# Performance work log

Measured on AMD Instinct MI355X. Metric: run time of the kernel, lower is better.

The kernel has to match this reference:

```python
import math
import jax, jax.numpy as jnp
import numpy as np

D_MODEL = 256
NUM_HEAD = 8
NUM_LEVEL = 1
KERNEL = 5
NUM_POINT = KERNEL * KERNEL
NUM_VAR = 5  # with_rotation=True
HEAD_DIM = D_MODEL // NUM_HEAD


def _kernel_indices(k=KERNEL):
    # odd kernel: linspace(-(k-1)/2, (k-1)/2, k); torch.meshgrid default 'ij'; stack([j,i])/k
    idx = jnp.linspace(-(k - 1) / 2.0, (k - 1) / 2.0, k)
    ii, jj = jnp.meshgrid(idx, idx, indexing='ij')
    return jnp.stack([jj, ii], axis=-1).reshape(-1, 2) / k  # (P, 2)


def setup_inputs() -> dict:
    key = jax.random.key(0)
    ks = jax.random.split(key, 8)
    B, LQ = 2, 4096
    Hf, Wf = 188, 188
    LV = Hf * Wf
    d = D_MODEL
    nb = NUM_LEVEL * NUM_HEAD * NUM_VAR
    na = NUM_HEAD * NUM_LEVEL * NUM_POINT
    return {
        'query': jax.random.normal(ks[0], (B, LQ, d), jnp.float32),
        'value': jax.random.normal(ks[1], (B, LV, d), jnp.float32),
        'ref_windows': jax.random.uniform(ks[2], (B, LQ, 7), jnp.float32),
        'W_box': jax.random.normal(ks[3], (nb, d), jnp.float32) * 0.02,
        'b_box': jax.random.uniform(ks[4], (nb,), jnp.float32),
        'W_attn': jax.random.normal(ks[5], (na, d), jnp.float32) * 0.02,
        'b_attn': jnp.zeros((na,), jnp.float32),
        'W_value': jax.random.normal(ks[6], (d, d), jnp.float32) * 0.02,
        'b_value': jnp.zeros((d,), jnp.float32),
        'W_out': jax.random.normal(ks[7], (d, d), jnp.float32) * 0.02,
        'b_out': jnp.zeros((d,), jnp.float32),
        'H_feat': Hf,
        'W_feat': Wf,
    }


def reference(query, value, ref_windows, W_box, b_box, W_attn, b_attn,
              W_value, b_value, W_out, b_out, H_feat, W_feat):
    B, LQ, d = query.shape
    LV = value.shape[1]
    Hh, Lv, P, Dh = NUM_HEAD, NUM_LEVEL, NUM_POINT, HEAD_DIM

    # value projection -> (B, LV, Hh, Dh)
    v = (value @ W_value.T + b_value).reshape(B, LV, Hh, Dh)

    # attention weights: softmax over (level*point) per head
    attn = jax.nn.softmax((query @ W_attn.T + b_attn).reshape(B, LQ, Hh, Lv * P), axis=-1)
    attn = attn.reshape(B, LQ, Hh, Lv, P)

    # --- _where_to_attend ---
    ob = (query @ W_box.T + b_box).reshape(B, LQ, Hh, Lv, NUM_VAR)
    rw = ref_windows[:, :, None, None, :]                    # (B,LQ,1,1,7)
    ref_boxes = rw[..., jnp.array([0, 1, 3, 4])]             # cx, cy, w, h
    ref_angles = rw[..., 6:7]
    off_boxes, off_angles = ob[..., :4], ob[..., 4:5]
    angles = (ref_angles + off_angles / 16.0) * (2.0 * math.pi)
    boxes = ref_boxes + off_boxes / 8.0 * ref_boxes[..., jnp.array([2, 3, 2, 3])]
    center = boxes[..., None, :2]                            # (B,LQ,Hh,Lv,1,2)
    size = boxes[..., None, 2:4]
    cos_a, sin_a = jnp.cos(angles), jnp.sin(angles)
    rot = jnp.stack([cos_a, -sin_a, sin_a, cos_a], axis=-1).reshape(B, LQ, Hh, Lv, 1, 2, 2)
    g = _kernel_indices() * jax.nn.relu(size)                # (B,LQ,Hh,Lv,P,2)
    grid = center + (g[..., None, :] * rot).sum(-1)          # (B,LQ,Hh,Lv,P,2), normalized [0,1]

    # --- single-level bilinear sampling (align_corners=False, zero padding) ---
    gl = grid[:, :, :, 0]                                    # (B,LQ,Hh,P,2)
    gx = gl[..., 0] * W_feat - 0.5
    gy = gl[..., 1] * H_feat - 0.5
    x0 = jnp.floor(gx)
    y0 = jnp.floor(gy)
    x0i = x0.astype(jnp.int32)
    y0i = y0.astype(jnp.int32)
    wx1 = gx - x0
    wy1 = gy - y0
    wx0 = 1.0 - wx1
    wy0 = 1.0 - wy1

    b_idx = jnp.arange(B)[:, None, None, None]
    h_idx = jnp.arange(Hh)[None, None, :, None]

    def gather(yi, xi):
        valid = (xi >= 0) & (xi < W_feat) & (yi >= 0) & (yi < H_feat)
        lin = jnp.clip(yi, 0, H_feat - 1) * W_feat + jnp.clip(xi, 0, W_feat - 1)
        return v[b_idx, lin, h_idx] * valid[..., None]       # (B,LQ,Hh,P,Dh)

    s = (gather(y0i, x0i) * (wy0 * wx0)[..., None]
         + gather(y0i, x0i + 1) * (wy0 * wx1)[..., None]
         + gather(y0i + 1, x0i) * (wy1 * wx0)[..., None]
         + gather(y0i + 1, x0i + 1) * (wy1 * wx1)[..., None])

    out_heads = (s * attn[:, :, :, 0, :, None]).sum(axis=3)  # (B,LQ,Hh,Dh)
    out = out_heads.reshape(B, LQ, Hh * Dh) @ W_out.T + b_out
    attn_w = attn.reshape(B, LQ, Hh, Lv, KERNEL, KERNEL)
    return out, attn_w
```

## Files before the change

### kernel.cpp

```cpp
#include <hip/hip_runtime.h>


typedef float floatx4 __attribute__((ext_vector_type(4)));
typedef short shortx8 __attribute__((ext_vector_type(8)));

static __device__ __forceinline__ unsigned short f2bf(float x) {
    unsigned int u = __float_as_uint(x);
    return (unsigned short)((u + 0x7fffu + ((u >> 16) & 1u)) >> 16);
}
static __device__ __forceinline__ unsigned int pack2(float a, float b) {
    return (unsigned int)f2bf(a) | ((unsigned int)f2bf(b) << 16);
}
static __device__ __forceinline__ void async16(const void* g, void* lds) {
    __builtin_amdgcn_global_load_lds(
        (const __attribute__((address_space(1))) unsigned int*)g,
        (__attribute__((address_space(3))) unsigned int*)lds, 16, 0, 0);
}

__global__ __launch_bounds__(256) void convert_kernel(
    const float* __restrict__ W_value, unsigned short* __restrict__ wvbf,
    const float* __restrict__ W_attn, const float* __restrict__ W_box,
    float* __restrict__ Wab,
    const float* __restrict__ W_out, unsigned short* __restrict__ wobf,
    const float* __restrict__ b_attn, const float* __restrict__ b_box,
    float* __restrict__ bab)
{
    const int blk = blockIdx.x, tid = threadIdx.x;
    if (blk < 16) {
        int base = blk * 1024 + tid;
#pragma unroll
        for (int k = 0; k < 4; ++k) {
            int j = base + k * 256;
            float4 f = ((const float4*)W_value)[j];
            ((uint2*)wvbf)[j] = make_uint2(pack2(f.x, f.y), pack2(f.z, f.w));
        }
    } else if (blk < 32) {
        int base = (blk - 16) * 1024 + tid;
#pragma unroll
        for (int k = 0; k < 4; ++k) {
            int j = base + k * 256;
            int row = j >> 6, col = (j & 63) * 4;
            float4 f;
            if (row < 200)      f = *(const float4*)(W_attn + (size_t)row * 256 + col);
            else if (row < 240) f = *(const float4*)(W_box + (size_t)(row - 200) * 256 + col);
            else                f = make_float4(0.f, 0.f, 0.f, 0.f);
            ((float4*)Wab)[j] = f;
        }
    } else if (blk < 48) {
        int base = (blk - 32) * 1024 + tid;
#pragma unroll
        for (int k = 0; k < 4; ++k) {
            int j = base + k * 256;
            float4 f = ((const float4*)W_out)[j];
            ((uint2*)wobf)[j] = make_uint2(pack2(f.x, f.y), pack2(f.z, f.w));
        }
    } else {
        bab[tid] = tid < 200 ? b_attn[tid] : (tid < 240 ? b_box[tid - 200] : 0.f);
    }
}

template <int OUTMODE, int AFP32, int BM>
__global__ __launch_bounds__(256) void gemm_bf16(
    const void* __restrict__ Av,
    const unsigned short* __restrict__ Bw,
    const float* __restrict__ bias,
    void* __restrict__ Cv, int M, int LV)
{
    constexpr int NI = BM / 32;
    constexpr int TI = BM / 32;
    __shared__ unsigned short As[BM * 64];
    __shared__ unsigned short Bs[128 * 64];
    const int tid = threadIdx.x;
    const int wv = tid >> 6, lane = tid & 63;
    const int lr = lane & 15, lq = lane >> 4;
    const int m0 = blockIdx.x * BM, n0 = blockIdx.y * 128;
    const int wm = wv & 1, wn = wv >> 1;
    const int srow = tid >> 3;
    const int scol = (tid & 7) * 8;

    floatx4 acc[TI][4];
#pragma unroll
    for (int i = 0; i < TI; ++i)
#pragma unroll
        for (int j = 0; j < 4; ++j) acc[i][j] = (floatx4){0.f, 0.f, 0.f, 0.f};

    for (int kc = 0; kc < 4; ++kc) {
        const int k0 = kc * 64;
        __syncthreads();
#pragma unroll
        for (int i = 0; i < 4; ++i) {
            int rb = n0 + i * 32 + srow;
            async16(Bw + (size_t)rb * 256 + k0 + scol, (char*)Bs + i * 4096 + wv * 1024);
        }
        if constexpr (AFP32) {
            const float* Af = (const float*)Av;
#pragma unroll
            for (int i = 0; i < NI; ++i) {
                int ra = m0 + i * 32 + srow; ra = ra < M ? ra : M - 1;
                const float* ap = Af + (size_t)ra * 256 + k0 + scol;
                float4 f0 = *(const float4*)ap;
                float4 f1 = *(const float4*)(ap + 4);
                uint4 pv = make_uint4(pack2(f0.x, f0.y), pack2(f0.z, f0.w),
                                      pack2(f1.x, f1.y), pack2(f1.z, f1.w));
                *(uint4*)((char*)As + i * 4096 + wv * 1024 + lane * 16) = pv;
            }
        } else {
            const unsigned short* Ab = (const unsigned short*)Av;
#pragma unroll
            for (int i = 0; i < NI; ++i) {
                int ra = m0 + i * 32 + srow; ra = ra < M ? ra : M - 1;
                async16(Ab + (size_t)ra * 256 + k0 + scol, (char*)As + i * 4096 + wv * 1024);
            }
        }
        __syncthreads();
#pragma unroll
        for (int kk = 0; kk < 64; kk += 32) {
            shortx8 af[TI], bfr[4];
#pragma unroll
            for (int t = 0; t < TI; ++t)
                af[t]  = *(const shortx8*)&As[(wm * (BM / 2) + t * 16 + lr) * 64 + kk + lq * 8];
#pragma unroll
            for (int t = 0; t < 4; ++t)
                bfr[t] = *(const shortx8*)&Bs[(wn * 64 + t * 16 + lr) * 64 + kk + lq * 8];
#pragma unroll
            for (int ti = 0; ti < TI; ++ti)
#pragma unroll
                for (int tj = 0; tj < 4; ++tj)
                    acc[ti][tj] = __builtin_amdgcn_mfma_f32_16x16x32_bf16(bfr[tj], af[ti], acc[ti][tj], 0, 0, 0);
        }
    }
#pragma unroll
    for (int ti = 0; ti < TI; ++ti) {
        int m = m0 + wm * (BM / 2) + ti * 16 + lr;
        if (m >= M) continue;
        if (OUTMODE == 0) {
            float* Crow = (float*)Cv + (size_t)m * 256;
#pragma unroll
            for (int tj = 0; tj < 4; ++tj) {
                int nb = n0 + wn * 64 + tj * 16 + lq * 4;
                float4 bv = *(const float4*)(bias + nb);
                float4 o = make_float4(acc[ti][tj][0] + bv.x, acc[ti][tj][1] + bv.y,
                                       acc[ti][tj][2] + bv.z, acc[ti][tj][3] + bv.w);
                *(float4*)(Crow + nb) = o;
            }
        } else {
            int b = m >= LV ? 1 : 0;
            int lv = m - (b ? LV : 0);
#pragma unroll
            for (int tj = 0; tj < 4; ++tj) {
                int nb = n0 + wn * 64 + tj * 16 + lq * 4;
                float4 bv = *(const float4*)(bias + nb);
                int h = nb >> 5, dh = nb & 31;
                unsigned short* dst = (unsigned short*)Cv + ((size_t)(b * 8 + h) * LV + lv) * 32 + dh;
                *(uint2*)dst = make_uint2(pack2(acc[ti][tj][0] + bv.x, acc[ti][tj][1] + bv.y),
                                          pack2(acc[ti][tj][2] + bv.z, acc[ti][tj][3] + bv.w));
            }
        }
    }
}

__global__ __launch_bounds__(256) void gemm_nt_bias(
    const float* __restrict__ A, const float* __restrict__ W,
    const float* __restrict__ bias, float* __restrict__ C, int M)
{
    const int K = 256, N = 256;
    __shared__ float As[16][68];
    __shared__ float Bs[16][68];
    int tid = threadIdx.x;
    int tcol = tid & 15, trow = tid >> 4;
    int m0 = blockIdx.x * 64, n0 = blockIdx.y * 64;
    int lr = tid >> 2, lc = (tid & 3) << 2;
    float acc[4][4] = {};
    for (int k0 = 0; k0 < K; k0 += 16) {
        int arow = m0 + lr; if (arow > M - 1) arow = M - 1;
        float4 av = *(const float4*)(A + (size_t)arow * K + k0 + lc);
        float4 wv = *(const float4*)(W + (size_t)(n0 + lr) * K + k0 + lc);
        __syncthreads();
        As[lc + 0][lr] = av.x; As[lc + 1][lr] = av.y; As[lc + 2][lr] = av.z; As[lc + 3][lr] = av.w;
        Bs[lc + 0][lr] = wv.x; Bs[lc + 1][lr] = wv.y; Bs[lc + 2][lr] = wv.z; Bs[lc + 3][lr] = wv.w;
        __syncthreads();
#pragma unroll
        for (int k = 0; k < 16; ++k) {
            float4 a4 = *(const float4*)&As[k][trow << 2];
            float4 b4 = *(const float4*)&Bs[k][tcol << 2];
            float a[4] = {a4.x, a4.y, a4.z, a4.w};
            float bb[4] = {b4.x, b4.y, b4.z, b4.w};
#pragma unroll
            for (int i = 0; i < 4; i++)
#pragma unroll
                for (int j = 0; j < 4; j++) acc[i][j] += a[i] * bb[j];
        }
    }
#pragma unroll
    for (int i = 0; i < 4; i++) {
        int m = m0 + trow * 4 + i;
        if (m >= M) continue;
#pragma unroll
        for (int j = 0; j < 4; j++) {
            int n = n0 + tcol * 4 + j;
            C[(size_t)m * N + n] = acc[i][j] + bias[n];
        }
    }
}

__global__ __launch_bounds__(256) void decode_sample_kernel(
    const unsigned short* __restrict__ v,
    const float* __restrict__ logits,
    const float* __restrict__ ref_windows,
    float* __restrict__ attn_out,
    unsigned short* __restrict__ ohbf,
    const int* __restrict__ Hf_p, const int* __restrict__ Wf_p, int LV, int LQ)
{
    __shared__ float lg[8][32];
    __shared__ float rw[8][7];
    __shared__ float prm[8][6];
    __shared__ float mxinv[8][2];
    __shared__ uint4 pk[8][25][2];

    const int lin = blockIdx.y * 16 + blockIdx.x;
    const int nc = gridDim.y;
    const int seq = lin >> 3;
    const int c = seq % nc;
    const int s = (lin & 7) + ((seq / nc) << 3);
    const int b = s >> 3, h = s & 7;
    const int tid = threadIdx.x;
    const int Hf = *Hf_p, Wf = *Wf_p;
    const size_t mbase = (size_t)b * LQ + c * 8;

    if (tid < 240) {
        int qq = tid / 30, j = tid - qq * 30;
        int col = (j < 25) ? h * 25 + j : 200 + h * 5 + (j - 25);
        lg[qq][j] = logits[(mbase + qq) * 256 + col];
    }
    if (tid < 56) {
        int qq = tid / 7, k = tid - qq * 7;
        rw[qq][k] = ref_windows[(mbase + qq) * 7 + k];
    }
    __syncthreads();

    if (tid < 8) {
        int qq = tid;
        float mx = -1e30f;
#pragma unroll
        for (int p = 0; p < 25; p++) mx = fmaxf(mx, lg[qq][p]);
        float ssum = 0.f;
#pragma unroll
        for (int p = 0; p < 25; p++) ssum += expf(lg[qq][p] - mx);
        mxinv[qq][0] = mx; mxinv[qq][1] = 1.f / ssum;
        float cx = rw[qq][0] + lg[qq][25] * 0.125f * rw[qq][3];
        float cy = rw[qq][1] + lg[qq][26] * 0.125f * rw[qq][4];
        float bw = rw[qq][3] + lg[qq][27] * 0.125f * rw[qq][3];
        float bh = rw[qq][4] + lg[qq][28] * 0.125f * rw[qq][4];
        float ang = (rw[qq][6] + lg[qq][29] * 0.0625f) * 6.283185307179586f;
        prm[qq][0] = cx; prm[qq][1] = cy;
        prm[qq][2] = fmaxf(bw, 0.f); prm[qq][3] = fmaxf(bh, 0.f);
        prm[qq][4] = cosf(ang); prm[qq][5] = sinf(ang);
    }
    __syncthreads();

    if (tid < 200) {
        int qq = tid / 25, p = tid - qq * 25;
        float a = expf(lg[qq][p] - mxinv[qq][0]) * mxinv[qq][1];
        attn_out[(mbase + qq) * 200 + h * 25 + p] = a;
        int pi = p / 5, pj = p - pi * 5;
        float g0 = (float)(pj - 2) * 0.2f * prm[qq][2];
        float g1 = (float)(pi - 2) * 0.2f * prm[qq][3];
        float ca = prm[qq][4], sa = prm[qq][5];
        float gx = (prm[qq][0] + g0 * ca - g1 * sa) * (float)Wf - 0.5f;
        float gy = (prm[qq][1] + g0 * sa + g1 * ca) * (float)Hf - 0.5f;
        float x0f = floorf(gx), y0f = floorf(gy);
        int x0 = (int)x0f, y0 = (int)y0f;
        float wx1 = gx - x0f, wy1 = gy - y0f;
        float wx0 = 1.f - wx1, wy0 = 1.f - wy1;
        int y1 = y0 + 1;
        int bx; float wl, wr;
        if (x0 >= 0 && x0 <= Wf - 2)      { bx = x0;     wl = wx0; wr = wx1; }
        else if (x0 == -1)                { bx = 0;      wl = wx1; wr = 0.f; }
        else if (x0 == Wf - 1)            { bx = Wf - 2; wl = 0.f; wr = wx0; }
        else                              { bx = 0;      wl = 0.f; wr = 0.f; }
        float wy0v = (y0 >= 0 && y0 < Hf) ? wy0 : 0.f;
        float wy1v = (y1 >= 0 && y1 < Hf) ? wy1 : 0.f;
        int cy0 = min(max(y0, 0), Hf - 1), cy1 = min(max(y1, 0), Hf - 1);
        unsigned off0 = (unsigned)(cy0 * Wf + bx) * 16u;
        unsigned off1 = (unsigned)(cy1 * Wf + bx) * 16u;
        float aw0 = a * wy0v, aw1 = a * wy1v;
        pk[qq][p][0] = make_uint4(__float_as_uint(aw0 * wl), __float_as_uint(aw1 * wl), off0, off1);
        pk[qq][p][1] = make_uint4(__float_as_uint(aw0 * wr), __float_as_uint(aw1 * wr), off0, off1);
    }
    __syncthreads();

    const int qq = tid >> 5, l = tid & 31;
    const unsigned int* vw = (const unsigned int*)(v + (size_t)s * LV * 32);
    const uint4* pkp = &pk[qq][0][l >> 4];
    float e0 = 0.f, o0 = 0.f, e1 = 0.f, o1 = 0.f;
#pragma unroll
    for (int p = 0; p < 25; ++p) {
        uint4 t = pkp[2 * p];
        float w0 = __uint_as_float(t.x), w1 = __uint_as_float(t.y);
        unsigned u0 = vw[t.z + l];
        unsigned u1 = vw[t.w + l];
        e0 += w0 * __uint_as_float(u0 << 16);
        o0 += w0 * __uint_as_float(u0 & 0xffff0000u);
        e1 += w1 * __uint_as_float(u1 << 16);
        o1 += w1 * __uint_as_float(u1 & 0xffff0000u);
    }
    float a0 = e0 + e1, a1 = o0 + o1;
    a0 += __shfl_xor(a0, 16, 32);
    a1 += __shfl_xor(a1, 16, 32);
    if (l < 16)
        ((unsigned int*)ohbf)[(mbase + qq) * 128 + h * 16 + l] = pack2(a0, a1);
}

extern "C" void kernel_launch(void* const* d_in, const int* in_sizes, int n_in,
                              void* d_out, int out_size, void* d_ws, size_t ws_size,
                              hipStream_t stream) {
    const float* query       = (const float*)d_in[0];
    const float* value       = (const float*)d_in[1];
    const float* ref_windows = (const float*)d_in[2];
    const float* W_box       = (const float*)d_in[3];
    const float* b_box       = (const float*)d_in[4];
    const float* W_attn      = (const float*)d_in[5];
    const float* b_attn      = (const float*)d_in[6];
    const float* W_value     = (const float*)d_in[7];
    const float* b_value     = (const float*)d_in[8];
    const float* W_out       = (const float*)d_in[9];
    const float* b_out       = (const float*)d_in[10];
    const int*   Hf          = (const int*)d_in[11];
    const int*   Wf          = (const int*)d_in[12];

    const int M1 = in_sizes[1] / 256;
    const int MQ = in_sizes[0] / 256;
    const int LQ = MQ / 2;
    const int LV = M1 / 2;

    unsigned short* Vout = (unsigned short*)d_ws;
    unsigned short* ohbf = Vout + (size_t)M1 * 256;
    unsigned short* wvbf = ohbf + (size_t)MQ * 256;
    unsigned short* wobf = wvbf + 65536;
    float* Wab       = (float*)(wobf + 65536);
    float* bab       = Wab + 65536;
    float* logits    = bab + 256;

    float* out0     = (float*)d_out;
    float* attn_out = out0 + (size_t)MQ * 256;

    convert_kernel<<<49, 256, 0, stream>>>(W_value, wvbf, W_attn, W_box, Wab,
                                           W_out, wobf, b_attn, b_box, bab);
    dim3 g1((M1 + 127) / 128, 2);
    gemm_bf16<1, 1, 128><<<g1, 256, 0, stream>>>(value, wvbf, b_value, Vout, M1, LV);
    dim3 g2(MQ / 64, 4);
    gemm_nt_bias<<<g2, 256, 0, stream>>>(query, Wab, bab, logits, MQ);
    decode_sample_kernel<<<dim3(16, LQ / 8), 256, 0, stream>>>(
        Vout, logits, ref_windows, attn_out, ohbf, Hf, Wf, LV, LQ);
    dim3 g4(MQ / 64, 2);
    gemm_bf16<0, 0, 64><<<g4, 256, 0, stream>>>(ohbf, wobf, b_out, out0, MQ, LV);
}
```

Measured before the change: 215.3 us.

## Double-buffer GEMM LDS tiles and XOR-swizzle layout to avoid bank conflicts

The bf16 GEMM now keeps two LDS buffers for the A and B tiles. It prefetches the next K-chunk, using async global-to-LDS loads or register loads for fp32 A, while MFMAs run on the current chunk, which cuts one barrier per iteration. It also applies an XOR swizzle on 16-byte column groups, both on the stores into LDS and on the fragment reads, to reduce LDS bank conflicts. The cost is twice the LDS footprint, which may lower occupancy, and more registers held for prefetching fp32 A.

Measured after the change: 217.9 us. Within noise of the previous version (+1.2%).

```diff
diff --git a/kernel.cpp b/kernel.cpp
--- a/kernel.cpp
+++ b/kernel.cpp
@@ -68,15 +68,17 @@
 {
     constexpr int NI = BM / 32;
     constexpr int TI = BM / 32;
-    __shared__ unsigned short As[BM * 64];
-    __shared__ unsigned short Bs[128 * 64];
+    __shared__ unsigned short As[2][BM * 64];
+    __shared__ unsigned short Bs[2][128 * 64];
     const int tid = threadIdx.x;
     const int wv = tid >> 6, lane = tid & 63;
     const int lr = lane & 15, lq = lane >> 4;
     const int m0 = blockIdx.x * BM, n0 = blockIdx.y * 128;
     const int wm = wv & 1, wn = wv >> 1;
     const int srow = tid >> 3;
-    const int scol = (tid & 7) * 8;
+    const int colg = tid & 7;
+    const int colgSw = colg ^ (srow & 7);
+    const int dstA = (srow * 8 + colgSw) * 16;
 
     floatx4 acc[TI][4];
 #pragma unroll
@@ -84,50 +86,100 @@
 #pragma unroll
         for (int j = 0; j < 4; ++j) acc[i][j] = (floatx4){0.f, 0.f, 0.f, 0.f};
 
+    float4 ar0[NI], ar1[NI];
+
+    if constexpr (AFP32) {
+        const float* Af = (const float*)Av;
+#pragma unroll
+        for (int i = 0; i < NI; ++i) {
+            int ra = m0 + i * 32 + srow; ra = ra < M ? ra : M - 1;
+            const float* ap = Af + (size_t)ra * 256 + colg * 8;
+            ar0[i] = *(const float4*)ap;
+            ar1[i] = *(const float4*)(ap + 4);
+        }
+    } else {
+        const unsigned short* Ab = (const unsigned short*)Av;
+#pragma unroll
+        for (int i = 0; i < NI; ++i) {
+            int ra = m0 + i * 32 + srow; ra = ra < M ? ra : M - 1;
+            async16(Ab + (size_t)ra * 256 + colgSw * 8, (char*)As[0] + i * 4096 + wv * 1024);
+        }
+    }
+#pragma unroll
+    for (int i = 0; i < 4; ++i) {
+        int rb = n0 + i * 32 + srow;
+        async16(Bw + (size_t)rb * 256 + colgSw * 8, (char*)Bs[0] + i * 4096 + wv * 1024);
+    }
+    if constexpr (AFP32) {
+#pragma unroll
+        for (int i = 0; i < NI; ++i) {
+            uint4 pv = make_uint4(pack2(ar0[i].x, ar0[i].y), pack2(ar0[i].z, ar0[i].w),
+                                  pack2(ar1[i].x, ar1[i].y), pack2(ar1[i].z, ar1[i].w));
+            *(uint4*)((char*)As[0] + i * 4096 + dstA) = pv;
+        }
+    }
+    __syncthreads();
+
+    int cur = 0;
     for (int kc = 0; kc < 4; ++kc) {
-        const int k0 = kc * 64;
-        __syncthreads();
-#pragma unroll
-        for (int i = 0; i < 4; ++i) {
-            int rb = n0 + i * 32 + srow;
-            async16(Bw + (size_t)rb * 256 + k0 + scol, (char*)Bs + i * 4096 + wv * 1024);
-        }
-        if constexpr (AFP32) {
-            const float* Af = (const float*)Av;
-#pragma unroll
-            for (int i = 0; i < NI; ++i) {
-                int ra = m0 + i * 32 + srow; ra = ra < M ? ra : M - 1;
-                const float* ap = Af + (size_t)ra * 256 + k0 + scol;
-                float4 f0 = *(const float4*)ap;
-                float4 f1 = *(const float4*)(ap + 4);
-                uint4 pv = make_uint4(pack2(f0.x, f0.y), pack2(f0.z, f0.w),
-                                      pack2(f1.x, f1.y), pack2(f1.z, f1.w));
-                *(uint4*)((char*)As + i * 4096 + wv * 1024 + lane * 16) = pv;
-            }
-        } else {
-            const unsigned short* Ab = (const unsigned short*)Av;
-#pragma unroll
-            for (int i = 0; i < NI; ++i) {
-                int ra = m0 + i * 32 + srow; ra = ra < M ? ra : M - 1;
-                async16(Ab + (size_t)ra * 256 + k0 + scol, (char*)As + i * 4096 + wv * 1024);
-            }
-        }
-        __syncthreads();
-#pragma unroll
-        for (int kk = 0; kk < 64; kk += 32) {
+        const int nk = (kc + 1) * 64;
+        if (kc < 3) {
+            if constexpr (AFP32) {
+                const float* Af = (const float*)Av;
+#pragma unroll
+                for (int i = 0; i < NI; ++i) {
+                    int ra = m0 + i * 32 + srow; ra = ra < M ? ra : M - 1;
+                    const float* ap = Af + (size_t)ra * 256 + nk + colg * 8;
+                    ar0[i] = *(const float4*)ap;
+                    ar1[i] = *(const float4*)(ap + 4);
+                }
+            } else {
+                const unsigned short* Ab = (const unsigned short*)Av;
+#pragma unroll
+                for (int i = 0; i < NI; ++i) {
+                    int ra = m0 + i * 32 + srow; ra = ra < M ? ra : M - 1;
+                    async16(Ab + (size_t)ra * 256 + nk + colgSw * 8,
+                            (char*)As[cur ^ 1] + i * 4096 + wv * 1024);
+                }
+            }
+#pragma unroll
+            for (int i = 0; i < 4; ++i) {
+                int rb = n0 + i * 32 + srow;
+                async16(Bw + (size_t)rb * 256 + nk + colgSw * 8,
+                        (char*)Bs[cur ^ 1] + i * 4096 + wv * 1024);
+            }
+        }
+#pragma unroll
+        for (int kb = 0; kb < 2; ++kb) {
             shortx8 af[TI], bfr[4];
 #pragma unroll
-            for (int t = 0; t < TI; ++t)
-                af[t]  = *(const shortx8*)&As[(wm * (BM / 2) + t * 16 + lr) * 64 + kk + lq * 8];
-#pragma unroll
-            for (int t = 0; t < 4; ++t)
-                bfr[t] = *(const shortx8*)&Bs[(wn * 64 + t * 16 + lr) * 64 + kk + lq * 8];
+            for (int t = 0; t < TI; ++t) {
+                int arow = wm * (BM / 2) + t * 16 + lr;
+                af[t] = *(const shortx8*)&As[cur][arow * 64 + (((kb * 4 + lq) ^ (arow & 7)) * 8)];
+            }
+#pragma unroll
+            for (int t = 0; t < 4; ++t) {
+                int brow = wn * 64 + t * 16 + lr;
+                bfr[t] = *(const shortx8*)&Bs[cur][brow * 64 + (((kb * 4 + lq) ^ (brow & 7)) * 8)];
+            }
 #pragma unroll
             for (int ti = 0; ti < TI; ++ti)
 #pragma unroll
                 for (int tj = 0; tj < 4; ++tj)
                     acc[ti][tj] = __builtin_amdgcn_mfma_f32_16x16x32_bf16(bfr[tj], af[ti], acc[ti][tj], 0, 0, 0);
         }
+        if (kc < 3) {
+            if constexpr (AFP32) {
+#pragma unroll
+                for (int i = 0; i < NI; ++i) {
+                    uint4 pv = make_uint4(pack2(ar0[i].x, ar0[i].y), pack2(ar0[i].z, ar0[i].w),
+                                          pack2(ar1[i].x, ar1[i].y), pack2(ar1[i].z, ar1[i].w));
+                    *(uint4*)((char*)As[cur ^ 1] + i * 4096 + dstA) = pv;
+                }
+            }
+        }
+        __syncthreads();
+        cur ^= 1;
     }
 #pragma unroll
     for (int ti = 0; ti < TI; ++ti) {
```

## Replace LDS-staged bf16 GEMMs with direct global-to-register MFMA loads

Applied to the files above, without the earlier changes.

The bf16 MFMA GEMMs no longer stage A and B tiles through shared memory with async loads and barriers. Each lane now loads its MFMA fragments straight from global memory into registers. The value projection switches to 64x256 tiles so each block covers all output columns and the fp32 value rows are read and converted only once. This removes LDS traffic and __syncthreads stalls, but gives up intra-block operand reuse, relying on L1/L2 caching for the repeated weight reads, and issues more, narrower uncoalesced global loads.

After: 251.5 us. 16.8% more time.

```diff
diff --git a/kernel.cpp b/kernel.cpp
--- a/kernel.cpp
+++ b/kernel.cpp
@@ -10,11 +10,6 @@
 }
 static __device__ __forceinline__ unsigned int pack2(float a, float b) {
     return (unsigned int)f2bf(a) | ((unsigned int)f2bf(b) << 16);
-}
-static __device__ __forceinline__ void async16(const void* g, void* lds) {
-    __builtin_amdgcn_global_load_lds(
-        (const __attribute__((address_space(1))) unsigned int*)g,
-        (__attribute__((address_space(3))) unsigned int*)lds, 16, 0, 0);
 }
 
 __global__ __launch_bounds__(256) void convert_kernel(
@@ -59,76 +54,72 @@
     }
 }
 
-template <int OUTMODE, int AFP32, int BM>
-__global__ __launch_bounds__(256) void gemm_bf16(
+template <int OUTMODE, int AFP32, int BM, int BN>
+__global__ __launch_bounds__(256) void gemm_direct(
     const void* __restrict__ Av,
     const unsigned short* __restrict__ Bw,
     const float* __restrict__ bias,
     void* __restrict__ Cv, int M, int LV)
 {
-    constexpr int NI = BM / 32;
     constexpr int TI = BM / 32;
-    __shared__ unsigned short As[BM * 64];
-    __shared__ unsigned short Bs[128 * 64];
+    constexpr int TJ = BN / 32;
     const int tid = threadIdx.x;
     const int wv = tid >> 6, lane = tid & 63;
     const int lr = lane & 15, lq = lane >> 4;
-    const int m0 = blockIdx.x * BM, n0 = blockIdx.y * 128;
+    const int m0 = blockIdx.x * BM, n0 = blockIdx.y * BN;
     const int wm = wv & 1, wn = wv >> 1;
-    const int srow = tid >> 3;
-    const int scol = (tid & 7) * 8;
-
-    floatx4 acc[TI][4];
+
+    floatx4 acc[TI][TJ];
 #pragma unroll
     for (int i = 0; i < TI; ++i)
 #pragma unroll
-        for (int j = 0; j < 4; ++j) acc[i][j] = (floatx4){0.f, 0.f, 0.f, 0.f};
-
+        for (int j = 0; j < TJ; ++j) acc[i][j] = (floatx4){0.f, 0.f, 0.f, 0.f};
+
+    const float* apf[TI];
+    const unsigned short* apb[TI];
+#pragma unroll
+    for (int t = 0; t < TI; ++t) {
+        int ra = m0 + wm * (BM / 2) + t * 16 + lr; ra = ra < M ? ra : M - 1;
+        if constexpr (AFP32) apf[t] = (const float*)Av + (size_t)ra * 256 + lq * 8;
+        else                 apb[t] = (const unsigned short*)Av + (size_t)ra * 256 + lq * 8;
+    }
+    const unsigned short* bp[TJ];
+#pragma unroll
+    for (int t = 0; t < TJ; ++t) {
+        int rb = n0 + wn * (BN / 2) + t * 16 + lr;
+        bp[t] = Bw + (size_t)rb * 256 + lq * 8;
+    }
+
+#pragma unroll
     for (int kc = 0; kc < 4; ++kc) {
-        const int k0 = kc * 64;
-        __syncthreads();
-#pragma unroll
-        for (int i = 0; i < 4; ++i) {
-            int rb = n0 + i * 32 + srow;
-            async16(Bw + (size_t)rb * 256 + k0 + scol, (char*)Bs + i * 4096 + wv * 1024);
-        }
-        if constexpr (AFP32) {
-            const float* Af = (const float*)Av;
-#pragma unroll
-            for (int i = 0; i < NI; ++i) {
-                int ra = m0 + i * 32 + srow; ra = ra < M ? ra : M - 1;
-                const float* ap = Af + (size_t)ra * 256 + k0 + scol;
-                float4 f0 = *(const float4*)ap;
-                float4 f1 = *(const float4*)(ap + 4);
-                uint4 pv = make_uint4(pack2(f0.x, f0.y), pack2(f0.z, f0.w),
+#pragma unroll
+        for (int kb = 0; kb < 2; ++kb) {
+            const int ko = kc * 64 + kb * 32;
+            shortx8 af[TI], bfr[TJ];
+#pragma unroll
+            for (int t = 0; t < TJ; ++t)
+                bfr[t] = *(const shortx8*)(bp[t] + ko);
+#pragma unroll
+            for (int t = 0; t < TI; ++t) {
+                if constexpr (AFP32) {
+                    float4 f0 = *(const float4*)(apf[t] + ko);
+                    float4 f1 = *(const float4*)(apf[t] + ko + 4);
+                    union { uint4 u; shortx8 s; } cv;
+                    cv.u = make_uint4(pack2(f0.x, f0.y), pack2(f0.z, f0.w),
                                       pack2(f1.x, f1.y), pack2(f1.z, f1.w));
-                *(uint4*)((char*)As + i * 4096 + wv * 1024 + lane * 16) = pv;
+                    af[t] = cv.s;
+                } else {
+                    af[t] = *(const shortx8*)(apb[t] + ko);
+                }
             }
-        } else {
-            const unsigned short* Ab = (const unsigned short*)Av;
-#pragma unroll
-            for (int i = 0; i < NI; ++i) {
-                int ra = m0 + i * 32 + srow; ra = ra < M ? ra : M - 1;
-                async16(Ab + (size_t)ra * 256 + k0 + scol, (char*)As + i * 4096 + wv * 1024);
-            }
-        }
-        __syncthreads();
-#pragma unroll
-        for (int kk = 0; kk < 64; kk += 32) {
-            shortx8 af[TI], bfr[4];
-#pragma unroll
-            for (int t = 0; t < TI; ++t)
-                af[t]  = *(const shortx8*)&As[(wm * (BM / 2) + t * 16 + lr) * 64 + kk + lq * 8];
-#pragma unroll
-            for (int t = 0; t < 4; ++t)
-                bfr[t] = *(const shortx8*)&Bs[(wn * 64 + t * 16 + lr) * 64 + kk + lq * 8];
 #pragma unroll
             for (int ti = 0; ti < TI; ++ti)
 #pragma unroll
-                for (int tj = 0; tj < 4; ++tj)
+                for (int tj = 0; tj < TJ; ++tj)
                     acc[ti][tj] = __builtin_amdgcn_mfma_f32_16x16x32_bf16(bfr[tj], af[ti], acc[ti][tj], 0, 0, 0);
         }
     }
+
 #pragma unroll
     for (int ti = 0; ti < TI; ++ti) {
         int m = m0 + wm * (BM / 2) + ti * 16 + lr;
@@ -136,8 +127,8 @@
         if (OUTMODE == 0) {
             float* Crow = (float*)Cv + (size_t)m * 256;
 #pragma unroll
-            for (int tj = 0; tj < 4; ++tj) {
-                int nb = n0 + wn * 64 + tj * 16 + lq * 4;
+            for (int tj = 0; tj < TJ; ++tj) {
+                int nb = n0 + wn * (BN / 2) + tj * 16 + lq * 4;
                 float4 bv = *(const float4*)(bias + nb);
                 float4 o = make_float4(acc[ti][tj][0] + bv.x, acc[ti][tj][1] + bv.y,
                                        acc[ti][tj][2] + bv.z, acc[ti][tj][3] + bv.w);
@@ -147,8 +138,8 @@
             int b = m >= LV ? 1 : 0;
             int lv = m - (b ? LV : 0);
 #pragma unroll
-            for (int tj = 0; tj < 4; ++tj) {
-                int nb = n0 + wn * 64 + tj * 16 + lq * 4;
+            for (int tj = 0; tj < TJ; ++tj) {
+                int nb = n0 + wn * (BN / 2) + tj * 16 + lq * 4;
                 float4 bv = *(const float4*)(bias + nb);
                 int h = nb >> 5, dh = nb & 31;
                 unsigned short* dst = (unsigned short*)Cv + ((size_t)(b * 8 + h) * LV + lv) * 32 + dh;
@@ -346,12 +337,12 @@
 
     convert_kernel<<<49, 256, 0, stream>>>(W_value, wvbf, W_attn, W_box, Wab,
                                            W_out, wobf, b_attn, b_box, bab);
-    dim3 g1((M1 + 127) / 128, 2);
-    gemm_bf16<1, 1, 128><<<g1, 256, 0, stream>>>(value, wvbf, b_value, Vout, M1, LV);
+    dim3 g1((M1 + 63) / 64, 1);
+    gemm_direct<1, 1, 64, 256><<<g1, 256, 0, stream>>>(value, wvbf, b_value, Vout, M1, LV);
     dim3 g2(MQ / 64, 4);
     gemm_nt_bias<<<g2, 256, 0, stream>>>(query, Wab, bab, logits, MQ);
     decode_sample_kernel<<<dim3(16, LQ / 8), 256, 0, stream>>>(
         Vout, logits, ref_windows, attn_out, ohbf, Hf, Wf, LV, LQ);
-    dim3 g4(MQ / 64, 2);
-    gemm_bf16<0, 0, 64><<<g4, 256, 0, stream>>>(ohbf, wobf, b_out, out0, MQ, LV);
-}
+    dim3 g4((MQ + 63) / 64, 2);
+    gemm_direct<0, 0, 64, 128><<<g4, 256, 0, stream>>>(ohbf, wobf, b_out, out0, MQ, LV);
+}
```
